# Performance work log

Measured on AMD Instinct MI355X. Metric: run time of the kernel, lower is better.

## Reference

```python
import jax, jax.numpy as jnp
import numpy as np

B, C, H, W = 8, 288, 128, 128
CQ = C // 8  # 36


def setup_inputs() -> dict:
    key = jax.random.key(0)
    ks = jax.random.split(key, 9)
    s = 0.05
    return {
        "x": jax.random.normal(ks[0], (B, C, H, W), jnp.float32),
        "Wq": jax.random.normal(ks[1], (CQ, C), jnp.float32) * s,
        "bq": jax.random.normal(ks[2], (CQ,), jnp.float32) * s,
        "Wk": jax.random.normal(ks[3], (CQ, C), jnp.float32) * s,
        "bk": jax.random.normal(ks[4], (CQ,), jnp.float32) * s,
        "Wv": jax.random.normal(ks[5], (C, C), jnp.float32) * s,
        "bv": jax.random.normal(ks[6], (C,), jnp.float32) * s,
        "eca_w": jax.random.normal(ks[7], (3,), jnp.float32) * 0.5,
        "gamma": jax.random.normal(ks[8], (1,), jnp.float32),
    }


def reference(x, Wq, bq, Wk, bk, Wv, bv, eca_w, gamma):
    b, c, h, w = x.shape
    # 1x1 convs as channel GEMMs
    q = jnp.einsum('oc,bchw->bohw', Wq, x) + bq[None, :, None, None]
    k = jnp.einsum('oc,bchw->bohw', Wk, x) + bk[None, :, None, None]
    v = jnp.einsum('oc,bchw->bohw', Wv, x) + bv[None, :, None, None]

    # column (H-axis) scores with -inf diagonal mask: [b, h, w, h']
    eH = jnp.einsum('bchw,bcHw->bhwH', q, k)
    diag = jnp.eye(h, dtype=bool)[:, None, :]  # mask h == h'
    eH = jnp.where(diag, -jnp.inf, eH)
    # row (W-axis) scores: [b, h, w, w']
    eW = jnp.einsum('bchw,bchW->bhwW', q, k)

    # joint softmax over concatenated h' and w' axes
    att = jax.nn.softmax(jnp.concatenate([eH, eW], axis=-1), axis=-1)
    attH, attW = att[..., :h], att[..., h:]

    outH = jnp.einsum('bcHw,bhwH->bchw', v, attH)
    outW = jnp.einsum('bchW,bhwW->bchw', v, attW)

    # ECA channel attention (Conv1d over channel dim, kernel 3, pad 1, no bias)
    y = jnp.mean(x, axis=(2, 3))  # [b, c]
    yp = jnp.pad(y, ((0, 0), (1, 1)))
    yc = eca_w[0] * yp[:, :-2] + eca_w[1] * yp[:, 1:-1] + eca_w[2] * yp[:, 2:]
    chan = x * jax.nn.sigmoid(yc)[:, :, None, None]

    return gamma[0] * (outH + outW + chan) + x
```

## Files before the change

kernel.cpp:

```cpp
#include <hip/hip_runtime.h>
#include <hip/hip_bf16.h>


#define BB 8
#define CC 288
#define CQn 36
#define CQP 64
#define HH 128
#define WW 128
#define HWn (HH*WW)
#define MR 368

typedef __attribute__((ext_vector_type(8))) short bf16x8;
typedef __attribute__((ext_vector_type(4))) float f32x4;

static __device__ __forceinline__ unsigned short f2bf(float f) {
  __hip_bfloat16 h = __float2bfloat16(f);
  return __builtin_bit_cast(unsigned short, h);
}
static __device__ __forceinline__ float bf2f(unsigned short u) {
  unsigned int v = ((unsigned int)u) << 16;
  return __builtin_bit_cast(float, v);
}

__global__ void k_mean(const float* __restrict__ x, float* __restrict__ y) {
  int bc = blockIdx.x;
  const f32x4* p = (const f32x4*)(x + (size_t)bc * HWn);
  int t = threadIdx.x;
  float s = 0.f;
#pragma unroll
  for (int i = 0; i < 16; ++i) {
    f32x4 v = p[t + i * 256];
    s += v[0] + v[1] + v[2] + v[3];
  }
  s += __shfl_xor(s, 1);  s += __shfl_xor(s, 2);  s += __shfl_xor(s, 4);
  s += __shfl_xor(s, 8);  s += __shfl_xor(s, 16); s += __shfl_xor(s, 32);
  __shared__ float ls[4];
  if ((t & 63) == 0) ls[t >> 6] = s;
  __syncthreads();
  if (t == 0) y[bc] = (ls[0] + ls[1] + ls[2] + ls[3]) * (1.f / HWn);
}

__global__ void k_wcvt(const float* __restrict__ Wq, const float* __restrict__ Wk,
                       const float* __restrict__ Wv, const float* __restrict__ bq,
                       const float* __restrict__ bk, const float* __restrict__ bv,
                       unsigned short* __restrict__ Wcat, float* __restrict__ bcat) {
  int gid = blockIdx.x * 256 + threadIdx.x;
  int total = MR * CC;
  for (int i = gid; i < total; i += gridDim.x * 256) {
    int r = i / CC, c = i - r * CC;
    float v;
    if (r < 288) v = Wv[r * CC + c];
    else if (r < 324) v = Wq[(r - 288) * CC + c];
    else if (r < 360) v = Wk[(r - 324) * CC + c];
    else v = 0.f;
    Wcat[i] = f2bf(v);
  }
  if (gid < MR) {
    float bb;
    if (gid < 288) bb = bv[gid];
    else if (gid < 324) bb = bq[gid - 288];
    else if (gid < 360) bb = bk[gid - 324];
    else bb = 0.f;
    bcat[gid] = bb;
  }
}

__global__ void k_gate(const float* __restrict__ y, const float* __restrict__ eca,
                       float* __restrict__ gate) {
  int i = blockIdx.x * 256 + threadIdx.x;
  if (i >= BB * CC) return;
  int c = i % CC;
  float l = (c > 0)      ? y[i - 1] : 0.f;
  float r = (c < CC - 1) ? y[i + 1] : 0.f;
  float yc = eca[0] * l + eca[1] * y[i] + eca[2] * r;
  gate[i] = 1.f / (1.f + __expf(-yc));
}

__global__ __launch_bounds__(256, 2) void k_qkv(
    const float* __restrict__ x, const unsigned short* __restrict__ Wcat,
    const float* __restrict__ bcat,
    unsigned short* __restrict__ vstd, unsigned short* __restrict__ vT,
    unsigned short* __restrict__ qpix, unsigned short* __restrict__ kpix) {
  int blk = blockIdx.x;
  int b = blk >> 7, th = (blk >> 4) & 7, tw = blk & 15;
  int h0 = th * 16, w0 = tw * 8;
  int t = threadIdx.x;
  int lane = t & 63, wv = t >> 6;
  int l16 = lane & 15, lg = lane >> 4;

  __shared__ unsigned short xh[2][128][40];
  __shared__ unsigned short resg[96][136];

  f32x4 acc[23][2];
#pragma unroll
  for (int m = 0; m < 23; ++m) {
    acc[m][0] = {0.f, 0.f, 0.f, 0.f};
    acc[m][1] = {0.f, 0.f, 0.f, 0.f};
  }

  f32x4 ld[4];
  auto issue_loads = [&](int kc) {
#pragma unroll
    for (int i = 0; i < 4; ++i) {
      int qid = i * 256 + t;
      int c = qid >> 5, rem = qid & 31, hl = rem >> 1, wq = rem & 1;
      ld[i] = *(const f32x4*)(x + (((size_t)(b * CC + kc * 32 + c) * HH + h0 + hl) * WW + w0 + wq * 4));
    }
  };
  auto store_stage = [&](int buf) {
#pragma unroll
    for (int i = 0; i < 4; ++i) {
      int qid = i * 256 + t;
      int c = qid >> 5, rem = qid & 31, hl = rem >> 1, wq = rem & 1;
      int pb = hl * 8 + wq * 4;
#pragma unroll
      for (int e = 0; e < 4; ++e) {
        int p = pb + e;
        int cs = c ^ (((p >> 2) & 3) << 3);
        xh[buf][p][cs] = f2bf(ld[i][e]);
      }
    }
  };

  issue_loads(0);
  store_stage(0);
  __syncthreads();

  for (int kc = 0; kc < 9; ++kc) {
    if (kc < 8) issue_loads(kc + 1);
    int buf = kc & 1;
    bf16x8 bfr[2];
#pragma unroll
    for (int nt = 0; nt < 2; ++nt) {
      int p = (wv * 2 + nt) * 16 + l16;
      int coff = (lg * 8) ^ (((p >> 2) & 3) << 3);
      bfr[nt] = *(const bf16x8*)&xh[buf][p][coff];
    }
#pragma unroll
    for (int mt = 0; mt < 23; ++mt) {
      bf16x8 af = *(const bf16x8*)(Wcat + ((size_t)(mt * 16 + l16) * CC + kc * 32 + lg * 8));
      acc[mt][0] = __builtin_amdgcn_mfma_f32_16x16x32_bf16(af, bfr[0], acc[mt][0], 0, 0, 0);
      acc[mt][1] = __builtin_amdgcn_mfma_f32_16x16x32_bf16(af, bfr[1], acc[mt][1], 0, 0, 0);
    }
    if (kc < 8) store_stage(buf ^ 1);
    __syncthreads();
  }

#pragma unroll
  for (int chunk = 0; chunk < 3; ++chunk) {
    __syncthreads();
#pragma unroll
    for (int mi = 0; mi < 6; ++mi) {
      int mt = chunk * 6 + mi;
#pragma unroll
      for (int nt = 0; nt < 2; ++nt) {
        int n = (wv * 2 + nt) * 16 + l16;
#pragma unroll
        for (int j = 0; j < 4; ++j) {
          int ch = mt * 16 + lg * 4 + j;
          resg[mi * 16 + lg * 4 + j][n] = f2bf(acc[mt][nt][j] + bcat[ch]);
        }
      }
    }
    __syncthreads();
#pragma unroll
    for (int i = 0; i < 6; ++i) {
      int task = i * 256 + t;
      int cpr = task >> 4, hl = task & 15;
      uint4 val = *(const uint4*)&resg[cpr][hl * 8];
      int ch = chunk * 96 + cpr;
      *(uint4*)(vstd + (((size_t)(b * CC + ch) * HH + h0 + hl) * WW + w0)) = val;
    }
#pragma unroll
    for (int i = 0; i < 6; ++i) {
      int task = i * 256 + t;
      int cpr = task >> 4, wl = (task >> 1) & 7, hs = task & 1;
      unsigned int uu[4];
#pragma unroll
      for (int e2 = 0; e2 < 4; ++e2) {
        unsigned int lo = resg[cpr][(hs * 8 + 2 * e2) * 8 + wl];
        unsigned int hi = resg[cpr][(hs * 8 + 2 * e2 + 1) * 8 + wl];
        uu[e2] = lo | (hi << 16);
      }
      uint4 val; val.x = uu[0]; val.y = uu[1]; val.z = uu[2]; val.w = uu[3];
      int ch = chunk * 96 + cpr;
      *(uint4*)(vT + (((size_t)(b * WW + w0 + wl) * CC + ch) * HH + h0 + hs * 8)) = val;
    }
  }

  __syncthreads();
#pragma unroll
  for (int mi = 0; mi < 5; ++mi) {
    int mt = 18 + mi;
#pragma unroll
    for (int nt = 0; nt < 2; ++nt) {
      int n = (wv * 2 + nt) * 16 + l16;
#pragma unroll
      for (int j = 0; j < 4; ++j) {
        int rr = mi * 16 + lg * 4 + j;
        if (rr < 72) resg[rr][n] = f2bf(acc[mt][nt][j] + bcat[288 + rr]);
      }
    }
  }
  __syncthreads();
  {
    int px = t >> 1, tensor = t & 1;
    int hl = px >> 3, wl = px & 7;
    unsigned int uu[32];
#pragma unroll
    for (int e = 0; e < 32; ++e) {
      unsigned int lo = (2 * e < CQn)     ? (unsigned int)resg[tensor * CQn + 2 * e][px]     : 0u;
      unsigned int hi = (2 * e + 1 < CQn) ? (unsigned int)resg[tensor * CQn + 2 * e + 1][px] : 0u;
      uu[e] = lo | (hi << 16);
    }
    unsigned short* dst = (tensor ? kpix : qpix) +
                          ((size_t)((b * WW + w0 + wl) * HH + h0 + hl)) * CQP;
#pragma unroll
    for (int e2 = 0; e2 < 8; ++e2) {
      uint4 val; val.x = uu[e2 * 4]; val.y = uu[e2 * 4 + 1];
      val.z = uu[e2 * 4 + 2]; val.w = uu[e2 * 4 + 3];
      ((uint4*)dst)[e2] = val;
    }
  }
}

__global__ __launch_bounds__(256, 2) void k_stats(
    const unsigned short* __restrict__ qpix, const unsigned short* __restrict__ kpix,
    float* __restrict__ mout, float* __restrict__ sout, int variant) {
  int line = blockIdx.x;
  int b = line >> 7, r = line & 127;
  size_t qbase; int pstride;
  if (variant == 0) { qbase = (size_t)line * (HH * CQP); pstride = CQP; }
  else { qbase = (size_t)b * (WW * HH * CQP) + (size_t)r * CQP; pstride = HH * CQP; }
  const unsigned short* qb = qpix + qbase;
  const unsigned short* kb = kpix + qbase;
  int t = threadIdx.x, lane = t & 63, wv = t >> 6, l16 = lane & 15, lg = lane >> 4;

  f32x4 e[2][8];
#pragma unroll
  for (int pt = 0; pt < 2; ++pt)
#pragma unroll
    for (int Ht = 0; Ht < 8; ++Ht) e[pt][Ht] = {0.f, 0.f, 0.f, 0.f};

#pragma unroll
  for (int ks = 0; ks < 2; ++ks) {
    bf16x8 af[2];
#pragma unroll
    for (int pt = 0; pt < 2; ++pt)
      af[pt] = *(const bf16x8*)(qb + (size_t)((wv * 2 + pt) * 16 + l16) * pstride + ks * 32 + lg * 8);
#pragma unroll
    for (int Ht = 0; Ht < 8; ++Ht) {
      bf16x8 bfr = *(const bf16x8*)(kb + (size_t)(Ht * 16 + l16) * pstride + ks * 32 + lg * 8);
      e[0][Ht] = __builtin_amdgcn_mfma_f32_16x16x32_bf16(af[0], bfr, e[0][Ht], 0, 0, 0);
      e[1][Ht] = __builtin_amdgcn_mfma_f32_16x16x32_bf16(af[1], bfr, e[1][Ht], 0, 0, 0);
    }
  }

#pragma unroll
  for (int pt = 0; pt < 2; ++pt) {
    float mv[4], sv[4];
#pragma unroll
    for (int j = 0; j < 4; ++j) {
      int row = (wv * 2 + pt) * 16 + lg * 4 + j;
      float m = -3.0e38f;
#pragma unroll
      for (int Ht = 0; Ht < 8; ++Ht) {
        int col = Ht * 16 + l16;
        float ev = e[pt][Ht][j];
        if (variant == 0 && row == col) { ev = -1.0e30f; e[pt][Ht][j] = ev; }
        m = fmaxf(m, ev);
      }
      m = fmaxf(m, __shfl_xor(m, 1)); m = fmaxf(m, __shfl_xor(m, 2));
      m = fmaxf(m, __shfl_xor(m, 4)); m = fmaxf(m, __shfl_xor(m, 8));
      float s = 0.f;
#pragma unroll
      for (int Ht = 0; Ht < 8; ++Ht) s += __expf(e[pt][Ht][j] - m);
      s += __shfl_xor(s, 1); s += __shfl_xor(s, 2);
      s += __shfl_xor(s, 4); s += __shfl_xor(s, 8);
      mv[j] = m; sv[j] = s;
    }
    if (l16 == 0) {
#pragma unroll
      for (int j = 0; j < 4; ++j) {
        int row = (wv * 2 + pt) * 16 + lg * 4 + j;
        mout[(size_t)line * 128 + row] = mv[j];
        sout[(size_t)line * 128 + row] = sv[j];
      }
    }
  }
}

__global__ void k_comb(const float* __restrict__ mcol, const float* __restrict__ scol,
                       const float* __restrict__ mrow, const float* __restrict__ srow,
                       float* __restrict__ mf, float* __restrict__ rzf,
                       float* __restrict__ mg, float* __restrict__ rzg) {
  int idx = blockIdx.x * 256 + threadIdx.x;
  int b = idx >> 14;
  int hw = idx & 16383;
  int h = hw >> 7, w = hw & 127;
  int cidx = (b << 14) + (w << 7) + h;
  float mc = mcol[cidx], sc = scol[cidx];
  float mr = mrow[idx],  sr = srow[idx];
  float m = fmaxf(mc, mr);
  float Z = sc * __expf(mc - m) + sr * __expf(mr - m);
  float rz = 1.f / Z;
  mg[idx] = m;  rzg[idx] = rz;
  mf[cidx] = m; rzf[cidx] = rz;
}

__global__ __launch_bounds__(256, 2) void k_attout(
    const unsigned short* __restrict__ qpix, const unsigned short* __restrict__ kpix,
    const unsigned short* __restrict__ vsrc, unsigned short* __restrict__ outp,
    const float* __restrict__ mstat, const float* __restrict__ rzstat, int variant) {
  int line = blockIdx.x;
  int b = line >> 7, r = line & 127;
  size_t qbase, vbase; int pstride, vstride, ostride;
  if (variant == 0) {
    qbase = (size_t)line * (HH * CQP); pstride = CQP;
    vbase = (size_t)line * (CC * HH);  vstride = HH;  ostride = HH;
  } else {
    qbase = (size_t)b * (WW * HH * CQP) + (size_t)r * CQP; pstride = HH * CQP;
    vbase = (size_t)b * (CC * HWn) + (size_t)r * WW;       vstride = HWn; ostride = HWn;
  }
  const unsigned short* qb = qpix + qbase;
  const unsigned short* kb = kpix + qbase;
  const float* mb  = mstat  + (size_t)line * 128;
  const float* rzb = rzstat + (size_t)line * 128;
  int t = threadIdx.x, lane = t & 63, wv = t >> 6, l16 = lane & 15, lg = lane >> 4;

  __shared__ unsigned short attld[4][32][136];
  __shared__ unsigned short resg[4][48][40];

  f32x4 e[2][8];
#pragma unroll
  for (int pt = 0; pt < 2; ++pt)
#pragma unroll
    for (int Ht = 0; Ht < 8; ++Ht) e[pt][Ht] = {0.f, 0.f, 0.f, 0.f};
#pragma unroll
  for (int ks = 0; ks < 2; ++ks) {
    bf16x8 af[2];
#pragma unroll
    for (int pt = 0; pt < 2; ++pt)
      af[pt] = *(const bf16x8*)(qb + (size_t)((wv * 2 + pt) * 16 + l16) * pstride + ks * 32 + lg * 8);
#pragma unroll
    for (int Ht = 0; Ht < 8; ++Ht) {
      bf16x8 bfr = *(const bf16x8*)(kb + (size_t)(Ht * 16 + l16) * pstride + ks * 32 + lg * 8);
      e[0][Ht] = __builtin_amdgcn_mfma_f32_16x16x32_bf16(af[0], bfr, e[0][Ht], 0, 0, 0);
      e[1][Ht] = __builtin_amdgcn_mfma_f32_16x16x32_bf16(af[1], bfr, e[1][Ht], 0, 0, 0);
    }
  }

#pragma unroll
  for (int pt = 0; pt < 2; ++pt) {
#pragma unroll
    for (int j = 0; j < 4; ++j) {
      int rowg = (wv * 2 + pt) * 16 + lg * 4 + j;
      float m = mb[rowg], rz = rzb[rowg];
#pragma unroll
      for (int Ht = 0; Ht < 8; ++Ht) {
        int col = Ht * 16 + l16;
        float ev = e[pt][Ht][j];
        if (variant == 0 && rowg == col) ev = -1.0e30f;
        attld[wv][pt * 16 + lg * 4 + j][col] = f2bf(__expf(ev - m) * rz);
      }
    }
  }
  __syncthreads();

#pragma unroll
  for (int chunk = 0; chunk < 6; ++chunk) {
    f32x4 o[3][2];
#pragma unroll
    for (int mi = 0; mi < 3; ++mi) { o[mi][0] = {0.f,0.f,0.f,0.f}; o[mi][1] = {0.f,0.f,0.f,0.f}; }
#pragma unroll
    for (int kc = 0; kc < 4; ++kc) {
      bf16x8 bfr[2];
#pragma unroll
      for (int nt = 0; nt < 2; ++nt)
        bfr[nt] = *(const bf16x8*)&attld[wv][nt * 16 + l16][kc * 32 + lg * 8];
#pragma unroll
      for (int mi = 0; mi < 3; ++mi) {
        int mt = chunk * 3 + mi;
        bf16x8 af = *(const bf16x8*)(vsrc + vbase + (size_t)(mt * 16 + l16) * vstride + kc * 32 + lg * 8);
        o[mi][0] = __builtin_amdgcn_mfma_f32_16x16x32_bf16(af, bfr[0], o[mi][0], 0, 0, 0);
        o[mi][1] = __builtin_amdgcn_mfma_f32_16x16x32_bf16(af, bfr[1], o[mi][1], 0, 0, 0);
      }
    }
#pragma unroll
    for (int mi = 0; mi < 3; ++mi)
#pragma unroll
      for (int nt = 0; nt < 2; ++nt) {
        int nl = nt * 16 + l16;
#pragma unroll
        for (int j = 0; j < 4; ++j)
          resg[wv][mi * 16 + lg * 4 + j][nl] = f2bf(o[mi][nt][j]);
      }
    __syncthreads();
#pragma unroll
    for (int i = 0; i < 3; ++i) {
      int task = i * 64 + lane;
      int cpr = task >> 2, seg = task & 3;
      uint4 val = *(const uint4*)&resg[wv][cpr][seg * 8];
      int ch = chunk * 48 + cpr;
      *(uint4*)(outp + vbase + (size_t)ch * ostride + wv * 32 + seg * 8) = val;
    }
  }
}

__global__ void k_final(const unsigned short* __restrict__ outHT,
                        const unsigned short* __restrict__ outWs,
                        const float* __restrict__ x, const float* __restrict__ gate,
                        const float* __restrict__ gammap, float* __restrict__ out) {
  int blk = blockIdx.x;
  int b = blk / 1152;
  int rr = blk - b * 1152;
  int c = rr >> 2, h0 = (rr & 3) * 32;
  int t = threadIdx.x;
  __shared__ unsigned short ldsT[128][40];
#pragma unroll
  for (int i = 0; i < 2; ++i) {
    int task = i * 256 + t;
    int w = task >> 2, hq = task & 3;
    uint4 v = *(const uint4*)(outHT + ((size_t)(b * WW + w) * CC + c) * HH + h0 + hq * 8);
    *(uint4*)&ldsT[w][hq * 8] = v;
  }
  __syncthreads();
  float gm = gammap[0];
  float g = gate[b * CC + c];
  size_t rowbase = (size_t)(b * CC + c) * HH;
#pragma unroll
  for (int i = 0; i < 2; ++i) {
    int task = i * 256 + t;
    int hl = task >> 4, wq = task & 15;
    size_t goff = (rowbase + h0 + hl) * WW + wq * 8;
    uint4 ow4 = *(const uint4*)(outWs + goff);
    f32x4 x1 = *(const f32x4*)(x + goff);
    f32x4 x2 = *(const f32x4*)(x + goff + 4);
    unsigned int owu[4] = {ow4.x, ow4.y, ow4.z, ow4.w};
    f32x4 r1, r2;
#pragma unroll
    for (int e2 = 0; e2 < 8; ++e2) {
      float oh = bf2f(ldsT[wq * 8 + e2][hl]);
      unsigned int pair = owu[e2 >> 1];
      float ow = bf2f((unsigned short)((e2 & 1) ? (pair >> 16) : (pair & 0xffffu)));
      float xv = (e2 < 4) ? x1[e2 & 3] : x2[e2 & 3];
      float res = gm * (oh + ow + xv * g) + xv;
      if (e2 < 4) r1[e2 & 3] = res; else r2[e2 & 3] = res;
    }
    *(f32x4*)(out + goff) = r1;
    *(f32x4*)(out + goff + 4) = r2;
  }
}

extern "C" void kernel_launch(void* const* d_in, const int* in_sizes, int n_in,
                              void* d_out, int out_size, void* d_ws, size_t ws_size,
                              hipStream_t stream) {
  (void)in_sizes; (void)n_in; (void)out_size; (void)ws_size;
  const float* x     = (const float*)d_in[0];
  const float* Wq    = (const float*)d_in[1];
  const float* bq    = (const float*)d_in[2];
  const float* Wk    = (const float*)d_in[3];
  const float* bk    = (const float*)d_in[4];
  const float* Wv    = (const float*)d_in[5];
  const float* bv    = (const float*)d_in[6];
  const float* eca   = (const float*)d_in[7];
  const float* gamma = (const float*)d_in[8];
  float* out = (float*)d_out;

  char* p = (char*)d_ws;
  auto take = [&](size_t bytes) {
    char* r = p;
    p += (bytes + 255) & ~(size_t)255;
    return r;
  };
  unsigned short* qpix  = (unsigned short*)take((size_t)BB * HWn * CQP * 2);
  unsigned short* kpix  = (unsigned short*)take((size_t)BB * HWn * CQP * 2);
  unsigned short* vstd  = (unsigned short*)take((size_t)BB * CC * HWn * 2);
  unsigned short* vT    = (unsigned short*)take((size_t)BB * CC * HWn * 2);
  unsigned short* outHT = (unsigned short*)take((size_t)BB * CC * HWn * 2);
  unsigned short* outWs = (unsigned short*)take((size_t)BB * CC * HWn * 2);
  float* mcol = (float*)take((size_t)BB * HWn * 4);
  float* scol = (float*)take((size_t)BB * HWn * 4);
  float* mrow = (float*)take((size_t)BB * HWn * 4);
  float* srow = (float*)take((size_t)BB * HWn * 4);
  float* mf   = (float*)take((size_t)BB * HWn * 4);
  float* rzf  = (float*)take((size_t)BB * HWn * 4);
  float* mg   = (float*)take((size_t)BB * HWn * 4);
  float* rzg  = (float*)take((size_t)BB * HWn * 4);
  unsigned short* Wcat = (unsigned short*)take((size_t)MR * CC * 2);
  float* bcat = (float*)take((size_t)MR * 4);
  float* y    = (float*)take((size_t)BB * CC * 4);
  float* gate = (float*)take((size_t)BB * CC * 4);

  k_mean<<<dim3(BB * CC), dim3(256), 0, stream>>>(x, y);
  k_wcvt<<<dim3(128), dim3(256), 0, stream>>>(Wq, Wk, Wv, bq, bk, bv, Wcat, bcat);
  k_gate<<<dim3(9), dim3(256), 0, stream>>>(y, eca, gate);
  k_qkv<<<dim3(1024), dim3(256), 0, stream>>>(x, Wcat, bcat, vstd, vT, qpix, kpix);
  k_stats<<<dim3(1024), dim3(256), 0, stream>>>(qpix, kpix, mcol, scol, 0);
  k_stats<<<dim3(1024), dim3(256), 0, stream>>>(qpix, kpix, mrow, srow, 1);
  k_comb<<<dim3(512), dim3(256), 0, stream>>>(mcol, scol, mrow, srow, mf, rzf, mg, rzg);
  k_attout<<<dim3(1024), dim3(256), 0, stream>>>(qpix, kpix, vT, outHT, mf, rzf, 0);
  k_attout<<<dim3(1024), dim3(256), 0, stream>>>(qpix, kpix, vstd, outWs, mg, rzg, 1);
  k_final<<<dim3(BB * CC * 4), dim3(256), 0, stream>>>(outHT, outWs, x, gate, gamma, out);
}
```

Measured before the change: 795.5 us.

## Pretranspose x to pixel-major bf16 and retile QKV GEMM; separate V transpose

Adds a k_xT kernel that converts x to pixel-major bf16 and accumulates channel sums with atomics, replacing the separate mean kernel. The QKV projection is retiled into 128-row by 256-pixel tiles with 3 M-blocks and reads operands directly from global memory, so each wave reuses more operand data per MFMA. The vT transposed copy now comes from a dedicated k_vT kernel that reads vstd, and vT reuses the xpix buffer. The risks are an extra full pass over x, an extra pass over v, and the mean now being computed from bf16-rounded values.

```diff
diff --git a/kernel.cpp b/kernel.cpp
--- a/kernel.cpp
+++ b/kernel.cpp
@@ -9,7 +9,7 @@
 #define HH 128
 #define WW 128
 #define HWn (HH*WW)
-#define MR 368
+#define MR 384
 
 typedef __attribute__((ext_vector_type(8))) short bf16x8;
 typedef __attribute__((ext_vector_type(4))) float f32x4;
@@ -21,24 +21,6 @@
 static __device__ __forceinline__ float bf2f(unsigned short u) {
   unsigned int v = ((unsigned int)u) << 16;
   return __builtin_bit_cast(float, v);
-}
-
-__global__ void k_mean(const float* __restrict__ x, float* __restrict__ y) {
-  int bc = blockIdx.x;
-  const f32x4* p = (const f32x4*)(x + (size_t)bc * HWn);
-  int t = threadIdx.x;
-  float s = 0.f;
-#pragma unroll
-  for (int i = 0; i < 16; ++i) {
-    f32x4 v = p[t + i * 256];
-    s += v[0] + v[1] + v[2] + v[3];
-  }
-  s += __shfl_xor(s, 1);  s += __shfl_xor(s, 2);  s += __shfl_xor(s, 4);
-  s += __shfl_xor(s, 8);  s += __shfl_xor(s, 16); s += __shfl_xor(s, 32);
-  __shared__ float ls[4];
-  if ((t & 63) == 0) ls[t >> 6] = s;
-  __syncthreads();
-  if (t == 0) y[bc] = (ls[0] + ls[1] + ls[2] + ls[3]) * (1.f / HWn);
 }
 
 __global__ void k_wcvt(const float* __restrict__ Wq, const float* __restrict__ Wk,
@@ -66,163 +48,201 @@
   }
 }
 
+__global__ __launch_bounds__(256) void k_xT(const float* __restrict__ x,
+                                            unsigned short* __restrict__ xpix,
+                                            float* __restrict__ ysum) {
+  int blk = blockIdx.x;
+  int b = blk >> 8, px0 = (blk & 255) * 64;
+  int t = threadIdx.x;
+  __shared__ unsigned short lx[64][296];
+  const float* xb = x + (size_t)b * CC * HWn + px0;
+#pragma unroll
+  for (int i = 0; i < 18; ++i) {
+    int qid = i * 256 + t;
+    int c = qid >> 4, seg = qid & 15;
+    f32x4 v = *(const f32x4*)(xb + (size_t)c * HWn + seg * 4);
+#pragma unroll
+    for (int e = 0; e < 4; ++e) lx[seg * 4 + e][c] = f2bf(v[e]);
+  }
+  __syncthreads();
+  {
+    int px = t >> 2, part = t & 3;
+    unsigned short* dst = xpix + ((size_t)(b * HWn) + px0 + px) * CC + part * 72;
+    const uint4* src = (const uint4*)&lx[px][part * 72];
+#pragma unroll
+    for (int j = 0; j < 9; ++j) ((uint4*)dst)[j] = src[j];
+  }
+  for (int cc = t; cc < CC; cc += 256) {
+    float s = 0.f;
+#pragma unroll
+    for (int px = 0; px < 64; ++px) s += bf2f(lx[px][cc]);
+    atomicAdd(&ysum[b * CC + cc], s);
+  }
+}
+
 __global__ void k_gate(const float* __restrict__ y, const float* __restrict__ eca,
                        float* __restrict__ gate) {
   int i = blockIdx.x * 256 + threadIdx.x;
   if (i >= BB * CC) return;
   int c = i % CC;
-  float l = (c > 0)      ? y[i - 1] : 0.f;
-  float r = (c < CC - 1) ? y[i + 1] : 0.f;
-  float yc = eca[0] * l + eca[1] * y[i] + eca[2] * r;
+  const float sc = 1.f / HWn;
+  float l = (c > 0)      ? y[i - 1] * sc : 0.f;
+  float r = (c < CC - 1) ? y[i + 1] * sc : 0.f;
+  float yc = eca[0] * l + eca[1] * y[i] * sc + eca[2] * r;
   gate[i] = 1.f / (1.f + __expf(-yc));
 }
 
 __global__ __launch_bounds__(256, 2) void k_qkv(
-    const float* __restrict__ x, const unsigned short* __restrict__ Wcat,
+    const unsigned short* __restrict__ xpix, const unsigned short* __restrict__ Wcat,
     const float* __restrict__ bcat,
-    unsigned short* __restrict__ vstd, unsigned short* __restrict__ vT,
+    unsigned short* __restrict__ vstd,
     unsigned short* __restrict__ qpix, unsigned short* __restrict__ kpix) {
   int blk = blockIdx.x;
-  int b = blk >> 7, th = (blk >> 4) & 7, tw = blk & 15;
-  int h0 = th * 16, w0 = tw * 8;
+  int mb = blk % 3;
+  int nt = blk / 3;
+  int b = nt >> 6;
+  int pxb = (nt & 63) * 256;
+  int t = threadIdx.x, lane = t & 63, wv = t >> 6;
+  int wm = wv >> 1, wn = wv & 1;
+  int l16 = lane & 15, lg = lane >> 4;
+
+  const unsigned short* xb = xpix + ((size_t)b * HWn + pxb) * CC;
+  const unsigned short* wb = Wcat + (size_t)(mb * 128) * CC;
+
+  __shared__ unsigned short eps[72][280];
+
+  f32x4 acc[4][8];
+#pragma unroll
+  for (int mi = 0; mi < 4; ++mi)
+#pragma unroll
+    for (int ni = 0; ni < 8; ++ni) acc[mi][ni] = {0.f, 0.f, 0.f, 0.f};
+
+  for (int kc = 0; kc < 9; ++kc) {
+    int ko = kc * 32 + lg * 8;
+    bf16x8 af[4], bf[8];
+#pragma unroll
+    for (int mi = 0; mi < 4; ++mi)
+      af[mi] = *(const bf16x8*)(wb + (size_t)(wm * 64 + mi * 16 + l16) * CC + ko);
+#pragma unroll
+    for (int ni = 0; ni < 8; ++ni)
+      bf[ni] = *(const bf16x8*)(xb + (size_t)(wn * 128 + ni * 16 + l16) * CC + ko);
+#pragma unroll
+    for (int mi = 0; mi < 4; ++mi)
+#pragma unroll
+      for (int ni = 0; ni < 8; ++ni)
+        acc[mi][ni] = __builtin_amdgcn_mfma_f32_16x16x32_bf16(af[mi], bf[ni], acc[mi][ni], 0, 0, 0);
+  }
+
+#pragma unroll
+  for (int ch_i = 0; ch_i < 4; ++ch_i) {
+    int r0 = mb * 128 + ch_i * 32;
+    __syncthreads();
+    if (r0 < 288 && wm == (ch_i >> 1)) {
+      int mibase = (ch_i & 1) * 2;
+#pragma unroll
+      for (int mr = 0; mr < 2; ++mr) {
+#pragma unroll
+        for (int ni = 0; ni < 8; ++ni) {
+#pragma unroll
+          for (int j = 0; j < 4; ++j) {
+            int rrel = mr * 16 + lg * 4 + j;
+            eps[rrel][wn * 128 + ni * 16 + l16] =
+                f2bf(acc[mibase + mr][ni][j] + bcat[r0 + rrel]);
+          }
+        }
+      }
+    }
+    __syncthreads();
+    if (r0 < 288) {
+      int row = t >> 3, part = t & 7;
+      unsigned short* dst = vstd + (size_t)(b * CC + r0 + row) * HWn + pxb + part * 32;
+      const uint4* src = (const uint4*)&eps[row][part * 32];
+#pragma unroll
+      for (int j = 0; j < 4; ++j) ((uint4*)dst)[j] = src[j];
+    }
+  }
+
+  if (mb == 2) {
+    __syncthreads();
+    if (wm == 0) {
+#pragma unroll
+      for (int mr = 0; mr < 2; ++mr)
+#pragma unroll
+        for (int ni = 0; ni < 8; ++ni)
+#pragma unroll
+          for (int j = 0; j < 4; ++j) {
+            int rel = mr * 16 + lg * 4 + j;
+            eps[rel][wn * 128 + ni * 16 + l16] =
+                f2bf(acc[2 + mr][ni][j] + bcat[288 + rel]);
+          }
+    } else {
+#pragma unroll
+      for (int mi = 0; mi < 3; ++mi)
+#pragma unroll
+        for (int ni = 0; ni < 8; ++ni)
+#pragma unroll
+          for (int j = 0; j < 4; ++j) {
+            int rel = 32 + mi * 16 + lg * 4 + j;
+            if (rel < 72)
+              eps[rel][wn * 128 + ni * 16 + l16] =
+                  f2bf(acc[mi][ni][j] + bcat[288 + rel]);
+          }
+    }
+    __syncthreads();
+    {
+      int px = t;
+      int hl = px >> 7, w = px & 127;
+      int h = (pxb >> 7) + hl;
+      unsigned int uu[32];
+#pragma unroll
+      for (int e = 0; e < 18; ++e)
+        uu[e] = (unsigned int)eps[2 * e][px] | ((unsigned int)eps[2 * e + 1][px] << 16);
+#pragma unroll
+      for (int e = 18; e < 32; ++e) uu[e] = 0u;
+      unsigned short* dq = qpix + ((size_t)(b * WW + w) * HH + h) * CQP;
+#pragma unroll
+      for (int e2 = 0; e2 < 8; ++e2) {
+        uint4 val; val.x = uu[e2 * 4]; val.y = uu[e2 * 4 + 1];
+        val.z = uu[e2 * 4 + 2]; val.w = uu[e2 * 4 + 3];
+        ((uint4*)dq)[e2] = val;
+      }
+#pragma unroll
+      for (int e = 0; e < 18; ++e)
+        uu[e] = (unsigned int)eps[36 + 2 * e][px] | ((unsigned int)eps[37 + 2 * e][px] << 16);
+      unsigned short* dk = kpix + ((size_t)(b * WW + w) * HH + h) * CQP;
+#pragma unroll
+      for (int e2 = 0; e2 < 8; ++e2) {
+        uint4 val; val.x = uu[e2 * 4]; val.y = uu[e2 * 4 + 1];
+        val.z = uu[e2 * 4 + 2]; val.w = uu[e2 * 4 + 3];
+        ((uint4*)dk)[e2] = val;
+      }
+    }
+  }
+}
+
+__global__ __launch_bounds__(256) void k_vT(const unsigned short* __restrict__ vstd,
+                                            unsigned short* __restrict__ vT) {
+  int blk = blockIdx.x;
+  int b = blk / 576, r = blk - b * 576;
+  int c = r >> 1, wh = (r & 1) * 64;
   int t = threadIdx.x;
-  int lane = t & 63, wv = t >> 6;
-  int l16 = lane & 15, lg = lane >> 4;
-
-  __shared__ unsigned short xh[2][128][40];
-  __shared__ unsigned short resg[96][136];
-
-  f32x4 acc[23][2];
-#pragma unroll
-  for (int m = 0; m < 23; ++m) {
-    acc[m][0] = {0.f, 0.f, 0.f, 0.f};
-    acc[m][1] = {0.f, 0.f, 0.f, 0.f};
-  }
-
-  f32x4 ld[4];
-  auto issue_loads = [&](int kc) {
-#pragma unroll
-    for (int i = 0; i < 4; ++i) {
-      int qid = i * 256 + t;
-      int c = qid >> 5, rem = qid & 31, hl = rem >> 1, wq = rem & 1;
-      ld[i] = *(const f32x4*)(x + (((size_t)(b * CC + kc * 32 + c) * HH + h0 + hl) * WW + w0 + wq * 4));
-    }
-  };
-  auto store_stage = [&](int buf) {
-#pragma unroll
-    for (int i = 0; i < 4; ++i) {
-      int qid = i * 256 + t;
-      int c = qid >> 5, rem = qid & 31, hl = rem >> 1, wq = rem & 1;
-      int pb = hl * 8 + wq * 4;
-#pragma unroll
-      for (int e = 0; e < 4; ++e) {
-        int p = pb + e;
-        int cs = c ^ (((p >> 2) & 3) << 3);
-        xh[buf][p][cs] = f2bf(ld[i][e]);
-      }
-    }
-  };
-
-  issue_loads(0);
-  store_stage(0);
+  __shared__ unsigned short lv[64][136];
+  const unsigned short* src = vstd + (size_t)(b * CC + c) * HWn + wh;
+#pragma unroll
+  for (int i = 0; i < 4; ++i) {
+    int qid = i * 256 + t;
+    int h = qid >> 3, seg = qid & 7;
+    uint4 v = *(const uint4*)(src + (size_t)h * WW + seg * 8);
+    const unsigned short* pv = (const unsigned short*)&v;
+#pragma unroll
+    for (int e = 0; e < 8; ++e) lv[seg * 8 + e][h] = pv[e];
+  }
   __syncthreads();
-
-  for (int kc = 0; kc < 9; ++kc) {
-    if (kc < 8) issue_loads(kc + 1);
-    int buf = kc & 1;
-    bf16x8 bfr[2];
-#pragma unroll
-    for (int nt = 0; nt < 2; ++nt) {
-      int p = (wv * 2 + nt) * 16 + l16;
-      int coff = (lg * 8) ^ (((p >> 2) & 3) << 3);
-      bfr[nt] = *(const bf16x8*)&xh[buf][p][coff];
-    }
-#pragma unroll
-    for (int mt = 0; mt < 23; ++mt) {
-      bf16x8 af = *(const bf16x8*)(Wcat + ((size_t)(mt * 16 + l16) * CC + kc * 32 + lg * 8));
-      acc[mt][0] = __builtin_amdgcn_mfma_f32_16x16x32_bf16(af, bfr[0], acc[mt][0], 0, 0, 0);
-      acc[mt][1] = __builtin_amdgcn_mfma_f32_16x16x32_bf16(af, bfr[1], acc[mt][1], 0, 0, 0);
-    }
-    if (kc < 8) store_stage(buf ^ 1);
-    __syncthreads();
-  }
-
-#pragma unroll
-  for (int chunk = 0; chunk < 3; ++chunk) {
-    __syncthreads();
-#pragma unroll
-    for (int mi = 0; mi < 6; ++mi) {
-      int mt = chunk * 6 + mi;
-#pragma unroll
-      for (int nt = 0; nt < 2; ++nt) {
-        int n = (wv * 2 + nt) * 16 + l16;
-#pragma unroll
-        for (int j = 0; j < 4; ++j) {
-          int ch = mt * 16 + lg * 4 + j;
-          resg[mi * 16 + lg * 4 + j][n] = f2bf(acc[mt][nt][j] + bcat[ch]);
-        }
-      }
-    }
-    __syncthreads();
-#pragma unroll
-    for (int i = 0; i < 6; ++i) {
-      int task = i * 256 + t;
-      int cpr = task >> 4, hl = task & 15;
-      uint4 val = *(const uint4*)&resg[cpr][hl * 8];
-      int ch = chunk * 96 + cpr;
-      *(uint4*)(vstd + (((size_t)(b * CC + ch) * HH + h0 + hl) * WW + w0)) = val;
-    }
-#pragma unroll
-    for (int i = 0; i < 6; ++i) {
-      int task = i * 256 + t;
-      int cpr = task >> 4, wl = (task >> 1) & 7, hs = task & 1;
-      unsigned int uu[4];
-#pragma unroll
-      for (int e2 = 0; e2 < 4; ++e2) {
-        unsigned int lo = resg[cpr][(hs * 8 + 2 * e2) * 8 + wl];
-        unsigned int hi = resg[cpr][(hs * 8 + 2 * e2 + 1) * 8 + wl];
-        uu[e2] = lo | (hi << 16);
-      }
-      uint4 val; val.x = uu[0]; val.y = uu[1]; val.z = uu[2]; val.w = uu[3];
-      int ch = chunk * 96 + cpr;
-      *(uint4*)(vT + (((size_t)(b * WW + w0 + wl) * CC + ch) * HH + h0 + hs * 8)) = val;
-    }
-  }
-
-  __syncthreads();
-#pragma unroll
-  for (int mi = 0; mi < 5; ++mi) {
-    int mt = 18 + mi;
-#pragma unroll
-    for (int nt = 0; nt < 2; ++nt) {
-      int n = (wv * 2 + nt) * 16 + l16;
-#pragma unroll
-      for (int j = 0; j < 4; ++j) {
-        int rr = mi * 16 + lg * 4 + j;
-        if (rr < 72) resg[rr][n] = f2bf(acc[mt][nt][j] + bcat[288 + rr]);
-      }
-    }
-  }
-  __syncthreads();
-  {
-    int px = t >> 1, tensor = t & 1;
-    int hl = px >> 3, wl = px & 7;
-    unsigned int uu[32];
-#pragma unroll
-    for (int e = 0; e < 32; ++e) {
-      unsigned int lo = (2 * e < CQn)     ? (unsigned int)resg[tensor * CQn + 2 * e][px]     : 0u;
-      unsigned int hi = (2 * e + 1 < CQn) ? (unsigned int)resg[tensor * CQn + 2 * e + 1][px] : 0u;
-      uu[e] = lo | (hi << 16);
-    }
-    unsigned short* dst = (tensor ? kpix : qpix) +
-                          ((size_t)((b * WW + w0 + wl) * HH + h0 + hl)) * CQP;
-#pragma unroll
-    for (int e2 = 0; e2 < 8; ++e2) {
-      uint4 val; val.x = uu[e2 * 4]; val.y = uu[e2 * 4 + 1];
-      val.z = uu[e2 * 4 + 2]; val.w = uu[e2 * 4 + 3];
-      ((uint4*)dst)[e2] = val;
-    }
-  }
+  int w = t >> 2, part = t & 3;
+  unsigned short* dst = vT + ((size_t)(b * WW + wh + w) * CC + c) * HH + part * 32;
+  const uint4* srcl = (const uint4*)&lv[w][part * 32];
+#pragma unroll
+  for (int j = 0; j < 4; ++j) ((uint4*)dst)[j] = srcl[j];
 }
 
 __global__ __launch_bounds__(256, 2) void k_stats(
@@ -474,10 +494,10 @@
     p += (bytes + 255) & ~(size_t)255;
     return r;
   };
+  unsigned short* xpix  = (unsigned short*)take((size_t)BB * HWn * CC * 2);
   unsigned short* qpix  = (unsigned short*)take((size_t)BB * HWn * CQP * 2);
   unsigned short* kpix  = (unsigned short*)take((size_t)BB * HWn * CQP * 2);
   unsigned short* vstd  = (unsigned short*)take((size_t)BB * CC * HWn * 2);
-  unsigned short* vT    = (unsigned short*)take((size_t)BB * CC * HWn * 2);
   unsigned short* outHT = (unsigned short*)take((size_t)BB * CC * HWn * 2);
   unsigned short* outWs = (unsigned short*)take((size_t)BB * CC * HWn * 2);
   float* mcol = (float*)take((size_t)BB * HWn * 4);
@@ -492,11 +512,14 @@
   float* bcat = (float*)take((size_t)MR * 4);
   float* y    = (float*)take((size_t)BB * CC * 4);
   float* gate = (float*)take((size_t)BB * CC * 4);
-
-  k_mean<<<dim3(BB * CC), dim3(256), 0, stream>>>(x, y);
+  unsigned short* vT = xpix;
+
+  hipMemsetAsync(y, 0, (size_t)BB * CC * 4, stream);
   k_wcvt<<<dim3(128), dim3(256), 0, stream>>>(Wq, Wk, Wv, bq, bk, bv, Wcat, bcat);
+  k_xT<<<dim3(2048), dim3(256), 0, stream>>>(x, xpix, y);
   k_gate<<<dim3(9), dim3(256), 0, stream>>>(y, eca, gate);
-  k_qkv<<<dim3(1024), dim3(256), 0, stream>>>(x, Wcat, bcat, vstd, vT, qpix, kpix);
+  k_qkv<<<dim3(1536), dim3(256), 0, stream>>>(xpix, Wcat, bcat, vstd, qpix, kpix);
+  k_vT<<<dim3(4608), dim3(256), 0, stream>>>(vstd, vT);
   k_stats<<<dim3(1024), dim3(256), 0, stream>>>(qpix, kpix, mcol, scol, 0);
   k_stats<<<dim3(1024), dim3(256), 0, stream>>>(qpix, kpix, mrow, srow, 1);
   k_comb<<<dim3(512), dim3(256), 0, stream>>>(mcol, scol, mrow, srow, mf, rzf, mg, rzg);
```

After: 651.4 us. 1.22x faster.
